# Optimization experiments

Hardware: AMD Instinct MI355X
Metric: run time of the kernel (lower is better)

Reference implementation:

```python
import jax, jax.numpy as jnp
import numpy as np

D_MODEL = 1024
N_HEADS = 16
D_K = D_MODEL // N_HEADS
B, S = 2, 2048


def setup_inputs() -> dict:
    key = jax.random.key(0)
    ks = jax.random.split(key, 11)
    s = 1.0 / np.sqrt(D_MODEL)
    return {
        "q": jax.random.normal(ks[0], (B, S, D_MODEL), jnp.float32),
        "k": jax.random.normal(ks[1], (B, S, D_MODEL), jnp.float32),
        "v": jax.random.normal(ks[2], (B, S, D_MODEL), jnp.float32),
        "Wq": jax.random.normal(ks[3], (D_MODEL, D_MODEL), jnp.float32) * s,
        "bq": jnp.zeros((D_MODEL,), jnp.float32),
        "Wk": jax.random.normal(ks[4], (D_MODEL, D_MODEL), jnp.float32) * s,
        "bk": jnp.zeros((D_MODEL,), jnp.float32),
        "Wv": jax.random.normal(ks[5], (D_MODEL, D_MODEL), jnp.float32) * s,
        "bv": jnp.zeros((D_MODEL,), jnp.float32),
        "Wo": jax.random.normal(ks[6], (D_MODEL, D_MODEL), jnp.float32) * s,
        "bo": jnp.zeros((D_MODEL,), jnp.float32),
    }


def reference(q, k, v, Wq, bq, Wk, bk, Wv, bv, Wo, bo):
    b = q.shape[0]
    # linear projections then split heads: [b, s, d] -> [b, h, s, d_k]
    def proj(x, W, bias):
        y = jnp.einsum('bsd,ed->bse', x, W) + bias  # torch Linear: x @ W.T + b
        return y.reshape(b, -1, N_HEADS, D_K).transpose(0, 2, 1, 3)

    qh, kh, vh = proj(q, Wq, bq), proj(k, Wk, bk), proj(v, Wv, bv)
    scores = jnp.einsum('bhqd,bhkd->bhqk', qh, kh) / np.sqrt(D_K)
    attn = jax.nn.softmax(scores, axis=-1)  # dropout: identity (eval mode)
    x = jnp.einsum('bhqk,bhkd->bhqd', attn, vh)
    x = x.transpose(0, 2, 1, 3).reshape(b, -1, D_MODEL)
    return jnp.einsum('bsd,ed->bse', x, Wo) + bo
```

## Files before the change

### kernel.cpp

```cpp
#include <hip/hip_runtime.h>
#include <math.h>
#include <stdint.h>

#define DM 1024
#define NH 16
#define DKH 64
#define BB 2
#define SS 2048
#define MM (BB*SS)

typedef __bf16 bf16;
typedef __bf16 bf16x8 __attribute__((ext_vector_type(8)));
typedef float f32x4 __attribute__((ext_vector_type(4)));

#define MFMA16(a,b,c) __builtin_amdgcn_mfma_f32_16x16x32_bf16((a),(b),(c),0,0,0)

#define SOFTMAX_C 12.0f
#define QSCALE 0.1803368801111204f

__device__ static inline void g2l16(const void* g, void* l) {
  __builtin_amdgcn_global_load_lds(
      (const __attribute__((address_space(1))) unsigned int*)g,
      (__attribute__((address_space(3))) unsigned int*)l, 16, 0, 0);
}

__global__ __launch_bounds__(256) void cvt_all(
    const float* __restrict__ q, const float* __restrict__ k, const float* __restrict__ v,
    const float* __restrict__ wq, const float* __restrict__ wk,
    const float* __restrict__ wv, const float* __restrict__ wo,
    bf16* __restrict__ Xq, bf16* __restrict__ Xk, bf16* __restrict__ Xv,
    bf16* __restrict__ Wqb, bf16* __restrict__ Wkb, bf16* __restrict__ Wvb,
    bf16* __restrict__ Wob)
{
  const long i = (long)blockIdx.x * 256 + threadIdx.x;
  const float* src; bf16* dst; long off;
  if (i < 3L * 524288L) {
    const int a = (int)(i / 524288L);
    off = (i % 524288L) * 8;
    src = (a == 0) ? q : (a == 1) ? k : v;
    dst = (a == 0) ? Xq : (a == 1) ? Xk : Xv;
  } else {
    const long j = i - 3L * 524288L;
    const int a = (int)(j / 131072L);
    off = (j % 131072L) * 8;
    src = (a == 0) ? wq : (a == 1) ? wk : (a == 2) ? wv : wo;
    dst = (a == 0) ? Wqb : (a == 1) ? Wkb : (a == 2) ? Wvb : Wob;
  }
  float4 f0 = *(const float4*)(src + off);
  float4 f1 = *(const float4*)(src + off + 4);
  bf16x8 o;
  o[0] = (bf16)f0.x; o[1] = (bf16)f0.y; o[2] = (bf16)f0.z; o[3] = (bf16)f0.w;
  o[4] = (bf16)f1.x; o[5] = (bf16)f1.y; o[6] = (bf16)f1.z; o[7] = (bf16)f1.w;
  *(bf16x8*)(dst + off) = o;
}

template<int EP, int BN>
__device__ __forceinline__ void gemm_bt_body(
    const bf16* __restrict__ A, const bf16* __restrict__ W,
    const float* __restrict__ bias, void* __restrict__ Y, float scale)
{
  constexpr int NT = BN / 32;
  constexpr int PB = BN / 32;
  __shared__ __align__(16) char smem[16384 + BN * 128];
  const int tid = threadIdx.x;
  const int lane = tid & 63, w = tid >> 6;
  const int ln15 = lane & 15, q4 = lane >> 4;
  const int m0 = blockIdx.x * 128;
  const int n0 = blockIdx.y * BN;
  const int mhalf = (w >> 1) * 64, nhalf = (w & 1) * (BN / 2);

  const bf16* gA[4]; const bf16* gB[PB];
  char* lA[4]; char* lB[PB];
  #pragma unroll
  for (int p = 0; p < 4; ++p) {
    const int n = p * 256 + tid;
    const int row = n >> 3, u = n & 7;
    const int g = u ^ (row & 7);
    gA[p] = A + (size_t)(m0 + row) * DM + g * 8;
    lA[p] = smem + n * 16;
  }
  #pragma unroll
  for (int p = 0; p < PB; ++p) {
    const int n = p * 256 + tid;
    const int row = n >> 3, u = n & 7;
    const int g = u ^ (row & 7);
    gB[p] = W + (size_t)(n0 + row) * DM + g * 8;
    lB[p] = smem + 16384 + n * 16;
  }

  int aoff[4][2], boff[NT][2];
  #pragma unroll
  for (int mt = 0; mt < 4; ++mt) {
    const int row = mhalf + mt * 16 + ln15;
    #pragma unroll
    for (int kc = 0; kc < 2; ++kc)
      aoff[mt][kc] = (row * 8 + ((kc * 4 + q4) ^ (row & 7))) * 16;
  }
  #pragma unroll
  for (int nt = 0; nt < NT; ++nt) {
    const int row = nhalf + nt * 16 + ln15;
    #pragma unroll
    for (int kc = 0; kc < 2; ++kc)
      boff[nt][kc] = 16384 + (row * 8 + ((kc * 4 + q4) ^ (row & 7))) * 16;
  }

  f32x4 acc[4][NT] = {};

  for (int kt = 0; kt < DM; kt += 64) {
    __syncthreads();
    #pragma unroll
    for (int p = 0; p < 4; ++p) g2l16(gA[p] + kt, lA[p]);
    #pragma unroll
    for (int p = 0; p < PB; ++p) g2l16(gB[p] + kt, lB[p]);
    asm volatile("s_waitcnt vmcnt(0)" ::: "memory");
    __syncthreads();
    #pragma unroll
    for (int kc = 0; kc < 2; ++kc) {
      bf16x8 af[4];
      #pragma unroll
      for (int mt = 0; mt < 4; ++mt) af[mt] = *(const bf16x8*)(smem + aoff[mt][kc]);
      #pragma unroll
      for (int nt = 0; nt < NT; ++nt) {
        bf16x8 bfr = *(const bf16x8*)(smem + boff[nt][kc]);
        #pragma unroll
        for (int mt = 0; mt < 4; ++mt)
          acc[mt][nt] = MFMA16(af[mt], bfr, acc[mt][nt]);
      }
    }
  }

  #pragma unroll
  for (int nt = 0; nt < NT; ++nt) {
    const int col = n0 + nhalf + nt * 16 + ln15;
    const float bv = bias[col];
    #pragma unroll
    for (int mt = 0; mt < 4; ++mt) {
      #pragma unroll
      for (int r = 0; r < 4; ++r) {
        const int row = m0 + mhalf + mt * 16 + q4 * 4 + r;
        const float val = (acc[mt][nt][r] + bv) * scale;
        if (EP == 0) {
          ((float*)Y)[(size_t)row * DM + col] = val;
        } else {
          const int b = row >> 11, s = row & 2047;
          const int h = col >> 6, dk = col & 63;
          ((bf16*)Y)[(((size_t)(b * NH + h) * SS + s) * DKH) + dk] = (bf16)val;
        }
      }
    }
  }
}

__global__ __launch_bounds__(256) void gemm_qkv(
    const bf16* Xq, const bf16* Xk, const bf16* Xv,
    const bf16* Wq, const bf16* Wk, const bf16* Wv,
    const float* bq, const float* bk, const float* bv,
    bf16* qh, bf16* kh, bf16* vh)
{
  const int z = blockIdx.z;
  const bf16* A = (z == 0) ? Xq : (z == 1) ? Xk : Xv;
  const bf16* W = (z == 0) ? Wq : (z == 1) ? Wk : Wv;
  const float* bias = (z == 0) ? bq : (z == 1) ? bk : bv;
  bf16* Y = (z == 0) ? qh : (z == 1) ? kh : vh;
  const float scale = (z == 0) ? QSCALE : 1.0f;
  gemm_bt_body<1, 128>(A, W, bias, Y, scale);
}

__global__ __launch_bounds__(256) void gemm_out(
    const bf16* A, const bf16* W, const float* bias, float* Y)
{
  gemm_bt_body<0, 64>(A, W, bias, Y, 1.0f);
}

__global__ __launch_bounds__(256) void transpose_v(
    const bf16* __restrict__ vh, bf16* __restrict__ vth)
{
  __shared__ unsigned short Ls[64][66];
  const int bh = blockIdx.y;
  const int s0 = blockIdx.x * 64;
  const int tid = threadIdx.x;
  const unsigned short* src = (const unsigned short*)(vh + (size_t)bh * SS * DKH);
  unsigned short* dst = (unsigned short*)(vth + (size_t)bh * SS * DKH);
  #pragma unroll
  for (int p = 0; p < 2; ++p) {
    const int n = p * 256 + tid;
    const int sl = n >> 3, dc = (n & 7) * 8;
    uint4 a = *(const uint4*)(src + (size_t)(s0 + sl) * DKH + dc);
    Ls[sl][dc + 0] = (unsigned short)(a.x & 0xffff);
    Ls[sl][dc + 1] = (unsigned short)(a.x >> 16);
    Ls[sl][dc + 2] = (unsigned short)(a.y & 0xffff);
    Ls[sl][dc + 3] = (unsigned short)(a.y >> 16);
    Ls[sl][dc + 4] = (unsigned short)(a.z & 0xffff);
    Ls[sl][dc + 5] = (unsigned short)(a.z >> 16);
    Ls[sl][dc + 6] = (unsigned short)(a.w & 0xffff);
    Ls[sl][dc + 7] = (unsigned short)(a.w >> 16);
  }
  __syncthreads();
  #pragma unroll
  for (int p = 0; p < 2; ++p) {
    const int n = p * 256 + tid;
    const int dk = n >> 3, sc = (n & 7) * 8;
    uint4 o;
    o.x = (unsigned)Ls[sc + 0][dk] | ((unsigned)Ls[sc + 1][dk] << 16);
    o.y = (unsigned)Ls[sc + 2][dk] | ((unsigned)Ls[sc + 3][dk] << 16);
    o.z = (unsigned)Ls[sc + 4][dk] | ((unsigned)Ls[sc + 5][dk] << 16);
    o.w = (unsigned)Ls[sc + 6][dk] | ((unsigned)Ls[sc + 7][dk] << 16);
    *(uint4*)(dst + (size_t)dk * SS + s0 + sc) = o;
  }
}

__global__ __launch_bounds__(256) void attn_mfma(
    const bf16* __restrict__ Qh, const bf16* __restrict__ Kh,
    const bf16* __restrict__ Vth, bf16* __restrict__ Xout)
{
  __shared__ __align__(16) char smem[51200];
  const int tid = threadIdx.x, lane = tid & 63, w = tid >> 6;
  const int ln15 = lane & 15, q4 = lane >> 4;
  const int bh = blockIdx.y, b = bh >> 4, h = bh & 15;
  const int q0 = blockIdx.x * 128 + w * 32;
  const bf16* Qb = Qh + (size_t)bh * SS * DKH;
  const bf16* Kb = Kh + (size_t)bh * SS * DKH;
  const bf16* Vb = Vth + (size_t)bh * SS * DKH;

  bf16x8 qf[2][2];
  #pragma unroll
  for (int mt = 0; mt < 2; ++mt)
    #pragma unroll
    for (int kc = 0; kc < 2; ++kc)
      qf[mt][kc] = *(const bf16x8*)(Qb + (size_t)(q0 + mt * 16 + ln15) * DKH + kc * 32 + q4 * 8);

  bf16x8 ones_frag;
  {
    const bf16 o = (ln15 == 0) ? (bf16)1.0f : (bf16)0.0f;
    #pragma unroll
    for (int j = 0; j < 8; ++j) ones_frag[j] = o;
  }

  const bf16* gK[2]; const bf16* gV[2];
  char* lK[2]; char* lV[2];
  #pragma unroll
  for (int p = 0; p < 2; ++p) {
    const int n = p * 256 + tid;
    const int row = n >> 3, u = n & 7;
    const int g = u ^ (row & 7);
    gK[p] = Kb + (size_t)row * DKH + g * 8;
    gV[p] = Vb + (size_t)row * SS + g * 8;
    lK[p] = smem + n * 16;
    lV[p] = smem + 8192 + n * 16;
  }
  char* Pl = smem + 32768 + w * 4608;

  int koff[4][2], voff[4][2], poff[2][2];
  #pragma unroll
  for (int nt = 0; nt < 4; ++nt) {
    const int rowi = nt * 16 + ln15;
    #pragma unroll
    for (int kc = 0; kc < 2; ++kc) {
      koff[nt][kc] = (rowi * 8 + ((kc * 4 + q4) ^ (rowi & 7))) * 16;
      voff[nt][kc] = 8192 + (rowi * 8 + ((kc * 4 + q4) ^ (rowi & 7))) * 16;
    }
  }
  #pragma unroll
  for (int mt = 0; mt < 2; ++mt)
    #pragma unroll
    for (int kc = 0; kc < 2; ++kc)
      poff[mt][kc] = ((mt * 16 + ln15) * 9 + kc * 4 + q4) * 16;

  f32x4 Oa[2][4] = {};
  f32x4 Ol[2] = {};

  #pragma unroll
  for (int p = 0; p < 2; ++p) {
    g2l16(gK[p], lK[p]); g2l16(gV[p], lV[p]);
    gK[p] += 64 * DKH; gV[p] += 64;
  }

  for (int kt = 0; kt < SS / 64; ++kt) {
    const int cur = (kt & 1) << 14;
    asm volatile("s_waitcnt vmcnt(0)" ::: "memory");
    __syncthreads();
    if (kt < SS / 64 - 1) {
      const int nxt = (~kt & 1) << 14;
      #pragma unroll
      for (int p = 0; p < 2; ++p) {
        g2l16(gK[p], lK[p] + nxt); g2l16(gV[p], lV[p] + nxt);
        gK[p] += 64 * DKH; gV[p] += 64;
      }
    }

    f32x4 S[2][4];
    #pragma unroll
    for (int mt = 0; mt < 2; ++mt)
      #pragma unroll
      for (int nt = 0; nt < 4; ++nt)
        S[mt][nt] = (f32x4){-SOFTMAX_C, -SOFTMAX_C, -SOFTMAX_C, -SOFTMAX_C};
    #pragma unroll
    for (int kc = 0; kc < 2; ++kc) {
      #pragma unroll
      for (int nt = 0; nt < 4; ++nt) {
        bf16x8 kf = *(const bf16x8*)(smem + cur + koff[nt][kc]);
        #pragma unroll
        for (int mt = 0; mt < 2; ++mt)
          S[mt][nt] = MFMA16(qf[mt][kc], kf, S[mt][nt]);
      }
    }

    #pragma unroll
    for (int mt = 0; mt < 2; ++mt)
      #pragma unroll
      for (int nt = 0; nt < 4; ++nt)
        #pragma unroll
        for (int r = 0; r < 4; ++r) {
          const int prow = mt * 16 + q4 * 4 + r;
          const int key = nt * 16 + ln15;
          *(bf16*)(Pl + prow * 144 + key * 2) =
              (bf16)__builtin_amdgcn_exp2f(S[mt][nt][r]);
        }
    asm volatile("s_waitcnt lgkmcnt(0)" ::: "memory");

    #pragma unroll
    for (int kc = 0; kc < 2; ++kc) {
      bf16x8 pf[2];
      #pragma unroll
      for (int mt = 0; mt < 2; ++mt) pf[mt] = *(const bf16x8*)(Pl + poff[mt][kc]);
      #pragma unroll
      for (int nt = 0; nt < 4; ++nt) {
        bf16x8 vf = *(const bf16x8*)(smem + cur + voff[nt][kc]);
        #pragma unroll
        for (int mt = 0; mt < 2; ++mt)
          Oa[mt][nt] = MFMA16(pf[mt], vf, Oa[mt][nt]);
      }
      #pragma unroll
      for (int mt = 0; mt < 2; ++mt)
        Ol[mt] = MFMA16(pf[mt], ones_frag, Ol[mt]);
    }
  }

  #pragma unroll
  for (int mt = 0; mt < 2; ++mt)
    #pragma unroll
    for (int r = 0; r < 4; ++r) {
      const float l = __shfl(Ol[mt][r], lane & 48);
      const float inv = 1.f / l;
      const int srow = q0 + mt * 16 + q4 * 4 + r;
      #pragma unroll
      for (int nt = 0; nt < 4; ++nt) {
        const int col = h * DKH + nt * 16 + ln15;
        Xout[((size_t)(b * SS + srow)) * DM + col] = (bf16)(Oa[mt][nt][r] * inv);
      }
    }
}

extern "C" void kernel_launch(void* const* d_in, const int* in_sizes, int n_in,
                              void* d_out, int out_size, void* d_ws, size_t ws_size,
                              hipStream_t stream)
{
  const float* q  = (const float*)d_in[0];
  const float* k  = (const float*)d_in[1];
  const float* v  = (const float*)d_in[2];
  const float* Wq = (const float*)d_in[3];
  const float* bq = (const float*)d_in[4];
  const float* Wk = (const float*)d_in[5];
  const float* bk = (const float*)d_in[6];
  const float* Wv = (const float*)d_in[7];
  const float* bv = (const float*)d_in[8];
  const float* Wo = (const float*)d_in[9];
  const float* bo = (const float*)d_in[10];
  float* out = (float*)d_out;

  char* ws = (char*)d_ws;
  const size_t MB = 1u << 20;
  bf16* Xq  = (bf16*)(ws + 0);
  bf16* Xk  = (bf16*)(ws + 8 * MB);
  bf16* Xv  = (bf16*)(ws + 16 * MB);
  bf16* Wqb = (bf16*)(ws + 24 * MB);
  bf16* Wkb = (bf16*)(ws + 26 * MB);
  bf16* Wvb = (bf16*)(ws + 28 * MB);
  bf16* Wob = (bf16*)(ws + 30 * MB);
  bf16* qh  = (bf16*)(ws + 32 * MB);
  bf16* kh  = (bf16*)(ws + 40 * MB);
  bf16* vh  = (bf16*)(ws + 48 * MB);
  bf16* vth = (bf16*)(ws + 56 * MB);
  bf16* xh  = Xq;

  cvt_all<<<8192, 256, 0, stream>>>(q, k, v, Wq, Wk, Wv, Wo,
                                    Xq, Xk, Xv, Wqb, Wkb, Wvb, Wob);

  gemm_qkv<<<dim3(32, 8, 3), 256, 0, stream>>>(Xq, Xk, Xv, Wqb, Wkb, Wvb,
                                               bq, bk, bv, qh, kh, vh);

  transpose_v<<<dim3(32, 32), 256, 0, stream>>>(vh, vth);

  attn_mfma<<<dim3(16, 32), 256, 0, stream>>>(qh, kh, vth, xh);

  gemm_out<<<dim3(32, 16), 256, 0, stream>>>(xh, Wob, bo, out);
}
```

Measured before the change: 218.4 us.

## Fuse V transpose into QKV GEMM epilogue and transpose attention MFMA roles

The V projection epilogue now writes directly in the transposed [b,h,dk,s] layout with 4-wide bf16 stores, removing the separate transpose_v kernel and its extra round-trip through global memory. In attention, the MFMA operand order is swapped (K·Q and V·P) so each lane holds four consecutive keys or head dims. That lets P be stored to LDS and the output written to global as packed bf16x4 rather than scalar bf16 stores. The row-sum now comes from an all-ones fragment without a shuffle. The GEMM epilogue ep selector became a runtime argument, which adds some branching.

```diff
diff --git a/kernel.cpp b/kernel.cpp
--- a/kernel.cpp
+++ b/kernel.cpp
@@ -11,6 +11,7 @@
 
 typedef __bf16 bf16;
 typedef __bf16 bf16x8 __attribute__((ext_vector_type(8)));
+typedef __bf16 bf16x4 __attribute__((ext_vector_type(4)));
 typedef float f32x4 __attribute__((ext_vector_type(4)));
 
 #define MFMA16(a,b,c) __builtin_amdgcn_mfma_f32_16x16x32_bf16((a),(b),(c),0,0,0)
@@ -54,10 +55,10 @@
   *(bf16x8*)(dst + off) = o;
 }
 
-template<int EP, int BN>
+template<int BN>
 __device__ __forceinline__ void gemm_bt_body(
     const bf16* __restrict__ A, const bf16* __restrict__ W,
-    const float* __restrict__ bias, void* __restrict__ Y, float scale)
+    const float* __restrict__ bias, void* __restrict__ Y, float scale, int ep)
 {
   constexpr int NT = BN / 32;
   constexpr int PB = BN / 32;
@@ -135,16 +136,26 @@
     const float bv = bias[col];
     #pragma unroll
     for (int mt = 0; mt < 4; ++mt) {
-      #pragma unroll
-      for (int r = 0; r < 4; ++r) {
-        const int row = m0 + mhalf + mt * 16 + q4 * 4 + r;
-        const float val = (acc[mt][nt][r] + bv) * scale;
-        if (EP == 0) {
-          ((float*)Y)[(size_t)row * DM + col] = val;
-        } else {
-          const int b = row >> 11, s = row & 2047;
-          const int h = col >> 6, dk = col & 63;
-          ((bf16*)Y)[(((size_t)(b * NH + h) * SS + s) * DKH) + dk] = (bf16)val;
+      if (ep == 2) {
+        const int s0 = m0 + mhalf + mt * 16 + q4 * 4;
+        const int b = s0 >> 11, s = s0 & 2047;
+        const int h = col >> 6, dk = col & 63;
+        bf16x4 pk;
+        #pragma unroll
+        for (int r = 0; r < 4; ++r) pk[r] = (bf16)(acc[mt][nt][r] + bv);
+        *(bf16x4*)((bf16*)Y + ((size_t)(b * NH + h) * DKH + dk) * SS + s) = pk;
+      } else {
+        #pragma unroll
+        for (int r = 0; r < 4; ++r) {
+          const int row = m0 + mhalf + mt * 16 + q4 * 4 + r;
+          const float val = (acc[mt][nt][r] + bv) * scale;
+          if (ep == 0) {
+            ((float*)Y)[(size_t)row * DM + col] = val;
+          } else {
+            const int b = row >> 11, s = row & 2047;
+            const int h = col >> 6, dk = col & 63;
+            ((bf16*)Y)[(((size_t)(b * NH + h) * SS + s) * DKH) + dk] = (bf16)val;
+          }
         }
       }
     }
@@ -155,58 +166,22 @@
     const bf16* Xq, const bf16* Xk, const bf16* Xv,
     const bf16* Wq, const bf16* Wk, const bf16* Wv,
     const float* bq, const float* bk, const float* bv,
-    bf16* qh, bf16* kh, bf16* vh)
+    bf16* qh, bf16* kh, bf16* vth)
 {
   const int z = blockIdx.z;
   const bf16* A = (z == 0) ? Xq : (z == 1) ? Xk : Xv;
   const bf16* W = (z == 0) ? Wq : (z == 1) ? Wk : Wv;
   const float* bias = (z == 0) ? bq : (z == 1) ? bk : bv;
-  bf16* Y = (z == 0) ? qh : (z == 1) ? kh : vh;
+  bf16* Y = (z == 0) ? qh : (z == 1) ? kh : vth;
   const float scale = (z == 0) ? QSCALE : 1.0f;
-  gemm_bt_body<1, 128>(A, W, bias, Y, scale);
+  const int ep = (z == 2) ? 2 : 1;
+  gemm_bt_body<128>(A, W, bias, Y, scale, ep);
 }
 
 __global__ __launch_bounds__(256) void gemm_out(
     const bf16* A, const bf16* W, const float* bias, float* Y)
 {
-  gemm_bt_body<0, 64>(A, W, bias, Y, 1.0f);
-}
-
-__global__ __launch_bounds__(256) void transpose_v(
-    const bf16* __restrict__ vh, bf16* __restrict__ vth)
-{
-  __shared__ unsigned short Ls[64][66];
-  const int bh = blockIdx.y;
-  const int s0 = blockIdx.x * 64;
-  const int tid = threadIdx.x;
-  const unsigned short* src = (const unsigned short*)(vh + (size_t)bh * SS * DKH);
-  unsigned short* dst = (unsigned short*)(vth + (size_t)bh * SS * DKH);
-  #pragma unroll
-  for (int p = 0; p < 2; ++p) {
-    const int n = p * 256 + tid;
-    const int sl = n >> 3, dc = (n & 7) * 8;
-    uint4 a = *(const uint4*)(src + (size_t)(s0 + sl) * DKH + dc);
-    Ls[sl][dc + 0] = (unsigned short)(a.x & 0xffff);
-    Ls[sl][dc + 1] = (unsigned short)(a.x >> 16);
-    Ls[sl][dc + 2] = (unsigned short)(a.y & 0xffff);
-    Ls[sl][dc + 3] = (unsigned short)(a.y >> 16);
-    Ls[sl][dc + 4] = (unsigned short)(a.z & 0xffff);
-    Ls[sl][dc + 5] = (unsigned short)(a.z >> 16);
-    Ls[sl][dc + 6] = (unsigned short)(a.w & 0xffff);
-    Ls[sl][dc + 7] = (unsigned short)(a.w >> 16);
-  }
-  __syncthreads();
-  #pragma unroll
-  for (int p = 0; p < 2; ++p) {
-    const int n = p * 256 + tid;
-    const int dk = n >> 3, sc = (n & 7) * 8;
-    uint4 o;
-    o.x = (unsigned)Ls[sc + 0][dk] | ((unsigned)Ls[sc + 1][dk] << 16);
-    o.y = (unsigned)Ls[sc + 2][dk] | ((unsigned)Ls[sc + 3][dk] << 16);
-    o.z = (unsigned)Ls[sc + 4][dk] | ((unsigned)Ls[sc + 5][dk] << 16);
-    o.w = (unsigned)Ls[sc + 6][dk] | ((unsigned)Ls[sc + 7][dk] << 16);
-    *(uint4*)(dst + (size_t)dk * SS + s0 + sc) = o;
-  }
+  gemm_bt_body<64>(A, W, bias, Y, 1.0f, 0);
 }
 
 __global__ __launch_bounds__(256) void attn_mfma(
@@ -224,17 +199,14 @@
 
   bf16x8 qf[2][2];
   #pragma unroll
-  for (int mt = 0; mt < 2; ++mt)
+  for (int qt = 0; qt < 2; ++qt)
     #pragma unroll
     for (int kc = 0; kc < 2; ++kc)
-      qf[mt][kc] = *(const bf16x8*)(Qb + (size_t)(q0 + mt * 16 + ln15) * DKH + kc * 32 + q4 * 8);
+      qf[qt][kc] = *(const bf16x8*)(Qb + (size_t)(q0 + qt * 16 + ln15) * DKH + kc * 32 + q4 * 8);
 
   bf16x8 ones_frag;
-  {
-    const bf16 o = (ln15 == 0) ? (bf16)1.0f : (bf16)0.0f;
-    #pragma unroll
-    for (int j = 0; j < 8; ++j) ones_frag[j] = o;
-  }
+  #pragma unroll
+  for (int j = 0; j < 8; ++j) ones_frag[j] = (bf16)1.0f;
 
   const bf16* gK[2]; const bf16* gV[2];
   char* lK[2]; char* lV[2];
@@ -250,7 +222,7 @@
   }
   char* Pl = smem + 32768 + w * 4608;
 
-  int koff[4][2], voff[4][2], poff[2][2];
+  int koff[4][2], voff[4][2], pst[4][2], pld[2][2];
   #pragma unroll
   for (int nt = 0; nt < 4; ++nt) {
     const int rowi = nt * 16 + ln15;
@@ -261,12 +233,17 @@
     }
   }
   #pragma unroll
-  for (int mt = 0; mt < 2; ++mt)
+  for (int k4 = 0; k4 < 4; ++k4)
+    #pragma unroll
+    for (int qt = 0; qt < 2; ++qt)
+      pst[k4][qt] = (qt * 16 + ln15) * 144 + (k4 * 16 + q4 * 4) * 2;
+  #pragma unroll
+  for (int qt = 0; qt < 2; ++qt)
     #pragma unroll
     for (int kc = 0; kc < 2; ++kc)
-      poff[mt][kc] = ((mt * 16 + ln15) * 9 + kc * 4 + q4) * 16;
-
-  f32x4 Oa[2][4] = {};
+      pld[qt][kc] = (qt * 16 + ln15) * 144 + kc * 64 + q4 * 16;
+
+  f32x4 Oa[4][2] = {};
   f32x4 Ol[2] = {};
 
   #pragma unroll
@@ -288,67 +265,66 @@
       }
     }
 
-    f32x4 S[2][4];
-    #pragma unroll
-    for (int mt = 0; mt < 2; ++mt)
-      #pragma unroll
-      for (int nt = 0; nt < 4; ++nt)
-        S[mt][nt] = (f32x4){-SOFTMAX_C, -SOFTMAX_C, -SOFTMAX_C, -SOFTMAX_C};
+    f32x4 St[4][2];
+    #pragma unroll
+    for (int k4 = 0; k4 < 4; ++k4)
+      #pragma unroll
+      for (int qt = 0; qt < 2; ++qt)
+        St[k4][qt] = (f32x4){-SOFTMAX_C, -SOFTMAX_C, -SOFTMAX_C, -SOFTMAX_C};
     #pragma unroll
     for (int kc = 0; kc < 2; ++kc) {
       #pragma unroll
-      for (int nt = 0; nt < 4; ++nt) {
-        bf16x8 kf = *(const bf16x8*)(smem + cur + koff[nt][kc]);
-        #pragma unroll
-        for (int mt = 0; mt < 2; ++mt)
-          S[mt][nt] = MFMA16(qf[mt][kc], kf, S[mt][nt]);
-      }
-    }
-
-    #pragma unroll
-    for (int mt = 0; mt < 2; ++mt)
-      #pragma unroll
-      for (int nt = 0; nt < 4; ++nt)
-        #pragma unroll
-        for (int r = 0; r < 4; ++r) {
-          const int prow = mt * 16 + q4 * 4 + r;
-          const int key = nt * 16 + ln15;
-          *(bf16*)(Pl + prow * 144 + key * 2) =
-              (bf16)__builtin_amdgcn_exp2f(S[mt][nt][r]);
-        }
+      for (int k4 = 0; k4 < 4; ++k4) {
+        bf16x8 kf = *(const bf16x8*)(smem + cur + koff[k4][kc]);
+        #pragma unroll
+        for (int qt = 0; qt < 2; ++qt)
+          St[k4][qt] = MFMA16(kf, qf[qt][kc], St[k4][qt]);
+      }
+    }
+
+    #pragma unroll
+    for (int k4 = 0; k4 < 4; ++k4)
+      #pragma unroll
+      for (int qt = 0; qt < 2; ++qt) {
+        bf16x4 pk;
+        #pragma unroll
+        for (int r = 0; r < 4; ++r)
+          pk[r] = (bf16)__builtin_amdgcn_exp2f(St[k4][qt][r]);
+        *(bf16x4*)(Pl + pst[k4][qt]) = pk;
+      }
     asm volatile("s_waitcnt lgkmcnt(0)" ::: "memory");
 
     #pragma unroll
     for (int kc = 0; kc < 2; ++kc) {
       bf16x8 pf[2];
       #pragma unroll
-      for (int mt = 0; mt < 2; ++mt) pf[mt] = *(const bf16x8*)(Pl + poff[mt][kc]);
-      #pragma unroll
-      for (int nt = 0; nt < 4; ++nt) {
-        bf16x8 vf = *(const bf16x8*)(smem + cur + voff[nt][kc]);
-        #pragma unroll
-        for (int mt = 0; mt < 2; ++mt)
-          Oa[mt][nt] = MFMA16(pf[mt], vf, Oa[mt][nt]);
-      }
-      #pragma unroll
-      for (int mt = 0; mt < 2; ++mt)
-        Ol[mt] = MFMA16(pf[mt], ones_frag, Ol[mt]);
-    }
-  }
-
-  #pragma unroll
-  for (int mt = 0; mt < 2; ++mt)
-    #pragma unroll
-    for (int r = 0; r < 4; ++r) {
-      const float l = __shfl(Ol[mt][r], lane & 48);
-      const float inv = 1.f / l;
-      const int srow = q0 + mt * 16 + q4 * 4 + r;
-      #pragma unroll
-      for (int nt = 0; nt < 4; ++nt) {
-        const int col = h * DKH + nt * 16 + ln15;
-        Xout[((size_t)(b * SS + srow)) * DM + col] = (bf16)(Oa[mt][nt][r] * inv);
-      }
-    }
+      for (int qt = 0; qt < 2; ++qt) pf[qt] = *(const bf16x8*)(Pl + pld[qt][kc]);
+      #pragma unroll
+      for (int dt = 0; dt < 4; ++dt) {
+        bf16x8 vf = *(const bf16x8*)(smem + cur + voff[dt][kc]);
+        #pragma unroll
+        for (int qt = 0; qt < 2; ++qt)
+          Oa[dt][qt] = MFMA16(vf, pf[qt], Oa[dt][qt]);
+      }
+      #pragma unroll
+      for (int qt = 0; qt < 2; ++qt)
+        Ol[qt] = MFMA16(ones_frag, pf[qt], Ol[qt]);
+    }
+  }
+
+  #pragma unroll
+  for (int qt = 0; qt < 2; ++qt) {
+    const float inv = 1.f / Ol[qt][0];
+    const int srow = q0 + qt * 16 + ln15;
+    bf16* dst = Xout + (size_t)(b * SS + srow) * DM + h * DKH + q4 * 4;
+    #pragma unroll
+    for (int dt = 0; dt < 4; ++dt) {
+      bf16x4 o4;
+      #pragma unroll
+      for (int r = 0; r < 4; ++r) o4[r] = (bf16)(Oa[dt][qt][r] * inv);
+      *(bf16x4*)(dst + dt * 16) = o4;
+    }
+  }
 }
 
 extern "C" void kernel_launch(void* const* d_in, const int* in_sizes, int n_in,
@@ -379,17 +355,14 @@
   bf16* Wob = (bf16*)(ws + 30 * MB);
   bf16* qh  = (bf16*)(ws + 32 * MB);
   bf16* kh  = (bf16*)(ws + 40 * MB);
-  bf16* vh  = (bf16*)(ws + 48 * MB);
-  bf16* vth = (bf16*)(ws + 56 * MB);
+  bf16* vth = (bf16*)(ws + 48 * MB);
   bf16* xh  = Xq;
 
   cvt_all<<<8192, 256, 0, stream>>>(q, k, v, Wq, Wk, Wv, Wo,
                                     Xq, Xk, Xv, Wqb, Wkb, Wvb, Wob);
 
   gemm_qkv<<<dim3(32, 8, 3), 256, 0, stream>>>(Xq, Xk, Xv, Wqb, Wkb, Wvb,
-                                               bq, bk, bv, qh, kh, vh);
-
-  transpose_v<<<dim3(32, 32), 256, 0, stream>>>(vh, vth);
+                                               bq, bk, bv, qh, kh, vth);
 
   attn_mfma<<<dim3(16, 32), 256, 0, stream>>>(qh, kh, vth, xh);
 
```

Result: no change. 222.5 us (+1.9%).
